# Kernel optimization log

Hardware: AMD Instinct MI355X
Metric: run time of the kernel (lower is better)

The kernel has to match this reference:

```python
import jax, jax.numpy as jnp
import numpy as np

NUM_HEADS = 8
GROUPS = 32
EPS = 1e-5


def setup_inputs() -> dict:
    key = jax.random.key(0)
    k1, k2, k3 = jax.random.split(key, 3)
    B, C, H, W = 16, 512, 64, 64
    x = jax.random.normal(k1, (B, C, H, W), dtype=jnp.float32)
    scale = C ** -0.5  # keep qkv/proj outputs well-scaled
    return {
        "x": x,
        "norm_w": jnp.ones((C,), jnp.float32),
        "norm_b": jnp.zeros((C,), jnp.float32),
        "qkv_w": jax.random.normal(k2, (3 * C, C), dtype=jnp.float32) * scale,
        "qkv_b": jnp.zeros((3 * C,), jnp.float32),
        "proj_w": jax.random.normal(k3, (C, C), dtype=jnp.float32) * scale,
        "proj_b": jnp.zeros((C,), jnp.float32),
    }


def reference(x, norm_w, norm_b, qkv_w, qkv_b, proj_w, proj_b):
    B, C, H, W = x.shape
    N = H * W
    nh = NUM_HEADS
    hd = C // nh

    # GroupNorm(32, C)
    xg = x.reshape(B, GROUPS, C // GROUPS, N)
    mu = xg.mean(axis=(2, 3), keepdims=True)
    var = xg.var(axis=(2, 3), keepdims=True)
    h = ((xg - mu) * jax.lax.rsqrt(var + EPS)).reshape(B, C, N)
    h = h * norm_w[None, :, None] + norm_b[None, :, None]

    h = h.transpose(0, 2, 1)  # [B, N, C]
    qkv = (h @ qkv_w.T + qkv_b).reshape(B, N, 3, nh, hd)
    q, k, v = qkv[:, :, 0], qkv[:, :, 1], qkv[:, :, 2]  # each [B, N, nh, hd]

    # Faithful to source: attention over the HEAD axis at each position
    attn = jnp.einsum('bnhd,bngd->bnhg', q, k) * (hd ** -0.5)  # [B, N, nh, nh]
    attn = jax.nn.softmax(attn, axis=-1)
    o = jnp.einsum('bnhg,bngd->bnhd', attn, v).reshape(B, N, C)

    o = o @ proj_w.T + proj_b  # [B, N, C]
    return x + o.transpose(0, 2, 1).reshape(B, C, H, W)
```

## Files before the change

kernel.cpp:

```cpp
#include <hip/hip_runtime.h>

typedef __attribute__((ext_vector_type(8))) short short8v;
typedef __attribute__((ext_vector_type(4))) float float4v;
typedef unsigned short ushortT;

__device__ __forceinline__ unsigned short f2bf(float f) {
  union { float f; unsigned u; } a; a.f = f;
  unsigned r = a.u + 0x7fffu + ((a.u >> 16) & 1u);
  return (unsigned short)(r >> 16);
}
__device__ __forceinline__ float2 up2(unsigned u) {
  union { unsigned u; float f; } a, b;
  a.u = u << 16; b.u = u & 0xffff0000u;
  return make_float2(a.f, b.f);
}
__device__ __forceinline__ void gl_lds16(const void* g, void* l) {
  __builtin_amdgcn_global_load_lds(
      (const __attribute__((address_space(1))) void*)g,
      (__attribute__((address_space(3))) void*)l, 16, 0, 0);
}

#define WAITV4 asm volatile("s_waitcnt vmcnt(4)" ::: "memory")
#define WAITV0 asm volatile("s_waitcnt vmcnt(0)" ::: "memory")
#define BAR()  __builtin_amdgcn_s_barrier()
#define MFMA16(d, a, b) d = __builtin_amdgcn_mfma_f32_16x16x32_bf16(a, b, d, 0, 0, 0)

__global__ __launch_bounds__(256) void prep(const float* __restrict__ qkvw,
                                            const float* __restrict__ pw,
                                            const float* __restrict__ x,
                                            ushortT* __restrict__ wq_b,
                                            ushortT* __restrict__ wp_b,
                                            float2* __restrict__ stats) {
  int bid = blockIdx.x, tid = threadIdx.x;
  if (bid < 1024) {
    const float* src = (bid < 768) ? qkvw : pw;
    ushortT* dst     = (bid < 768) ? wq_b : wp_b;
    int base = (bid < 768) ? bid : (bid - 768);
    int i = (base * 256 + tid) * 4;
    float4 v = *(const float4*)(src + i);
    uint2 o;
    o.x = (unsigned)f2bf(v.x) | ((unsigned)f2bf(v.y) << 16);
    o.y = (unsigned)f2bf(v.z) | ((unsigned)f2bf(v.w) << 16);
    *(uint2*)(dst + i) = o;
    return;
  }
  int bg = bid - 1024;
  const float* base = x + (size_t)bg * 65536;
  float s = 0.f, s2 = 0.f;
  for (int i = tid; i < 16384; i += 256) {
    float4 v = *(const float4*)(base + (size_t)i * 4);
    s  += v.x + v.y + v.z + v.w;
    s2 += v.x * v.x + v.y * v.y + v.z * v.z + v.w * v.w;
  }
  #pragma unroll
  for (int off = 32; off > 0; off >>= 1) {
    s  += __shfl_down(s, off);
    s2 += __shfl_down(s2, off);
  }
  __shared__ float red[8];
  int w = tid >> 6, l = tid & 63;
  if (l == 0) { red[w] = s; red[w + 4] = s2; }
  __syncthreads();
  if (tid == 0) {
    float ts = red[0] + red[1] + red[2] + red[3];
    float t2 = red[4] + red[5] + red[6] + red[7];
    float mean = ts * (1.f / 65536.f);
    float var  = t2 * (1.f / 65536.f) - mean * mean;
    stats[bg] = make_float2(mean, rsqrtf(var + 1e-5f));
  }
}

__global__ __launch_bounds__(512) void norm_tr(const float* __restrict__ x,
                                               const float* __restrict__ nw,
                                               const float* __restrict__ nb,
                                               const float2* __restrict__ stats,
                                               ushortT* __restrict__ h) {
  __shared__ float t[64][65];
  int n0 = blockIdx.x * 64, c0 = blockIdx.y * 64, b = blockIdx.z;
  int tx = threadIdx.x, ty = threadIdx.y;
  #pragma unroll
  for (int j = ty; j < 64; j += 8) {
    int c = c0 + j;
    float2 ms = stats[b * 32 + (c >> 4)];
    float v = x[((size_t)b * 512 + c) * 4096 + n0 + tx];
    t[j][tx] = (v - ms.x) * ms.y * nw[c] + nb[c];
  }
  __syncthreads();
  #pragma unroll
  for (int j = ty; j < 64; j += 8) {
    int n = n0 + j;
    h[((size_t)b * 4096 + n) * 512 + c0 + tx] = f2bf(t[tx][j]);
  }
}

__device__ __forceinline__ void core256b(const ushortT* __restrict__ A,
                                         const ushortT* __restrict__ Bm,
                                         ushortT* lds, int m0, int n0,
                                         float4v (&acc)[8][4]) {
  char* ldsb = (char*)lds;
  const int tid = threadIdx.x;
  const int w = tid >> 6, l = tid & 63;
  const int wm = w >> 2, wn = w & 3;

  const int P0b = tid * 16, P1b = 8192 + tid * 16;
  const int r0 = P0b >> 7, r1 = P1b >> 7;
  const int s0 = (P0b & 127) ^ ((r0 & 7) << 4);
  const int s1 = (P1b & 127) ^ ((r1 & 7) << 4);
  const size_t g0 = (size_t)r0 * 512 + (s0 >> 1);
  const size_t g1 = (size_t)r1 * 512 + (s1 >> 1);
  auto stage = [&](const ushortT* mat, int rowbase, int kt, int bufb, int region) {
    const ushortT* gsrc = mat + (size_t)rowbase * 512 + kt * 64;
    char* dbase = ldsb + bufb + region;
    gl_lds16(gsrc + g0, dbase + P0b);
    gl_lds16(gsrc + g1, dbase + P1b);
  };

  const int colb = (l >> 4) * 16;
  const int cs0 = colb ^ ((l & 7) << 4);
  const int cs1 = (64 + colb) ^ ((l & 7) << 4);
  const int arow = wm * 16384 + (l & 15) * 128;
  const int brow = 32768 + wn * 8192 + (l & 15) * 128;

  short8v Af[4][2], Bf[4][2];

  #define RDA4(bb, MH)                                                  \
    { _Pragma("unroll")                                                 \
      for (int mm = 0; mm < 4; ++mm) {                                  \
        const char* p = ldsb + (bb) + arow + ((MH)*4 + mm) * 2048;      \
        Af[mm][0] = *(const short8v*)(p + cs0);                         \
        Af[mm][1] = *(const short8v*)(p + cs1);                         \
      } }
  #define RDB2(bb, N0)                                                  \
    { _Pragma("unroll")                                                 \
      for (int nn = 0; nn < 2; ++nn) {                                  \
        const char* p = ldsb + (bb) + brow + ((N0) + nn) * 2048;        \
        Bf[(N0)+nn][0] = *(const short8v*)(p + cs0);                    \
        Bf[(N0)+nn][1] = *(const short8v*)(p + cs1);                    \
      } }
  #define CLUSTER(MH, NP)                                               \
    { __builtin_amdgcn_s_setprio(1);                                    \
      _Pragma("unroll")                                                 \
      for (int mm = 0; mm < 4; ++mm) {                                  \
        _Pragma("unroll")                                               \
        for (int nn = 0; nn < 2; ++nn) {                                \
          MFMA16(acc[(MH)*4+mm][(NP)*2+nn], Af[mm][0], Bf[(NP)*2+nn][0]); \
          MFMA16(acc[(MH)*4+mm][(NP)*2+nn], Af[mm][1], Bf[(NP)*2+nn][1]); \
        } }                                                             \
      __builtin_amdgcn_s_setprio(0); }

  auto tile = [&](int bb, int t1, int t2, bool s1g, bool s2g, int vw) {
    RDB2(bb, 0); RDA4(bb, 0);
    if (s1g) stage(A, m0 + 128, t1, bb ^ 65536, 16384);
    BAR();
    CLUSTER(0, 0);
    BAR();
    RDB2(bb, 2);
    if (s1g) stage(Bm, n0 + 128, t1, bb ^ 65536, 49152);
    BAR();
    CLUSTER(0, 1);
    BAR();
    RDA4(bb, 1);
    if (s2g) stage(Bm, n0, t2, bb, 32768);
    BAR();
    CLUSTER(1, 1);
    BAR();
    if (s2g) stage(A, m0, t2, bb, 0);
    if (vw == 4)      { WAITV4; }
    else if (vw == 0) { WAITV0; }
    BAR();
    CLUSTER(1, 0);
    BAR();
  };

  stage(A,  m0,       0, 0, 0);
  stage(A,  m0 + 128, 0, 0, 16384);
  stage(Bm, n0,       0, 0, 32768);
  stage(Bm, n0 + 128, 0, 0, 49152);
  stage(Bm, n0,       1, 65536, 32768);
  stage(A,  m0,       1, 65536, 0);
  WAITV4;
  BAR();

  #pragma unroll 1
  for (int tp = 0; tp < 3; ++tp) {
    tile(0,     2 * tp + 1, 2 * tp + 2, true, true, 4);
    tile(65536, 2 * tp + 2, 2 * tp + 3, true, true, 4);
  }
  tile(0,     7, 8, true,  false, 0);
  tile(65536, 8, 9, false, false, -1);
  #undef RDA4
  #undef RDB2
  #undef CLUSTER
}

__global__ __launch_bounds__(512, 2) void gemm_qkv(const ushortT* __restrict__ h,
                                                   const ushortT* __restrict__ wq,
                                                   const float* __restrict__ bias,
                                                   ushortT* __restrict__ outq) {
  __shared__ ushortT lds[65536];
  int bid = blockIdx.x;
  int wg = (bid & 7) * 192 + (bid >> 3);
  int m0 = (wg / 6) * 256, n0 = (wg % 6) * 256;
  float4v acc[8][4] = {};
  core256b(h, wq, lds, m0, n0, acc);
  const int tid = threadIdx.x;
  const int w = tid >> 6, l = tid & 63;
  const int wm = w >> 2, wn = w & 3;
  __syncthreads();
  ushortT* es = lds + w * 1280;
  float bb[4];
  #pragma unroll
  for (int fn = 0; fn < 4; ++fn) bb[fn] = bias[n0 + wn * 64 + fn * 16 + (l & 15)];
  int r = l >> 2, g = l & 3;
  #pragma unroll
  for (int fm = 0; fm < 8; ++fm) {
    #pragma unroll
    for (int fn = 0; fn < 4; ++fn)
      #pragma unroll
      for (int j = 0; j < 4; ++j)
        es[((l >> 4) * 4 + j) * 72 + fn * 16 + (l & 15)] = f2bf(acc[fm][fn][j] + bb[fn]);
    uint4 v0 = *(const uint4*)(es + r * 72 + g * 16);
    uint4 v1 = *(const uint4*)(es + r * 72 + g * 16 + 8);
    size_t mrow = (size_t)m0 + wm * 128 + fm * 16 + r;
    uint4* dst = (uint4*)(outq + mrow * 1536 + n0 + wn * 64 + g * 16);
    dst[0] = v0; dst[1] = v1;
  }
}

__global__ __launch_bounds__(256) void attn_k(const ushortT* __restrict__ qkv,
                                              ushortT* __restrict__ o) {
  __shared__ ushortT kv[16 * 1544];
  const int tid = threadIdx.x;
  const int p0 = blockIdx.x * 16;

  #pragma unroll
  for (int j = 0; j < 12; ++j) {
    int c = j * 256 + tid;
    int row = c / 192, col = c % 192;
    gl_lds16(qkv + (size_t)(p0 + row) * 1536 + col * 8,
             (char*)kv + row * 3088 + col * 16);
  }
  __syncthreads();

  const int pos = tid >> 4, h = (tid >> 1) & 7, dh = tid & 1;
  const ushortT* rowp = kv + pos * 1544;

  unsigned qv[16];
  {
    const uint4* qs = (const uint4*)(rowp + h * 64 + dh * 32);
    #pragma unroll
    for (int i = 0; i < 4; ++i) {
      uint4 u = qs[i];
      qv[i*4+0] = u.x; qv[i*4+1] = u.y; qv[i*4+2] = u.z; qv[i*4+3] = u.w;
    }
  }
  float lg[8];
  #pragma unroll
  for (int g = 0; g < 8; ++g) {
    const uint4* ks = (const uint4*)(rowp + 512 + g * 64 + dh * 32);
    float s = 0.f;
    #pragma unroll
    for (int i = 0; i < 4; ++i) {
      uint4 u = ks[i];
      float2 k0 = up2(u.x), k1 = up2(u.y), k2 = up2(u.z), k3 = up2(u.w);
      float2 q0 = up2(qv[i*4+0]), q1 = up2(qv[i*4+1]);
      float2 q2 = up2(qv[i*4+2]), q3 = up2(qv[i*4+3]);
      s += q0.x*k0.x + q0.y*k0.y + q1.x*k1.x + q1.y*k1.y
         + q2.x*k2.x + q2.y*k2.y + q3.x*k3.x + q3.y*k3.y;
    }
    s += __shfl_xor(s, 1);
    lg[g] = s * 0.125f;
  }
  float mx = lg[0];
  #pragma unroll
  for (int g = 1; g < 8; ++g) mx = fmaxf(mx, lg[g]);
  float ssum = 0.f;
  #pragma unroll
  for (int g = 0; g < 8; ++g) { lg[g] = __expf(lg[g] - mx); ssum += lg[g]; }
  float inv = 1.f / ssum;
  #pragma unroll
  for (int g = 0; g < 8; ++g) lg[g] *= inv;

  float oa[32];
  #pragma unroll
  for (int i = 0; i < 32; ++i) oa[i] = 0.f;
  #pragma unroll
  for (int g = 0; g < 8; ++g) {
    const uint4* vs = (const uint4*)(rowp + 1024 + g * 64 + dh * 32);
    float wg = lg[g];
    #pragma unroll
    for (int i = 0; i < 4; ++i) {
      uint4 u = vs[i];
      float2 v0 = up2(u.x), v1 = up2(u.y), v2 = up2(u.z), v3 = up2(u.w);
      oa[i*8+0] += wg*v0.x; oa[i*8+1] += wg*v0.y;
      oa[i*8+2] += wg*v1.x; oa[i*8+3] += wg*v1.y;
      oa[i*8+4] += wg*v2.x; oa[i*8+5] += wg*v2.y;
      oa[i*8+6] += wg*v3.x; oa[i*8+7] += wg*v3.y;
    }
  }
  ushortT* dst = o + (size_t)(p0 + pos) * 512 + h * 64 + dh * 32;
  #pragma unroll
  for (int i = 0; i < 4; ++i) {
    uint4 w_;
    w_.x = (unsigned)f2bf(oa[i*8+0]) | ((unsigned)f2bf(oa[i*8+1]) << 16);
    w_.y = (unsigned)f2bf(oa[i*8+2]) | ((unsigned)f2bf(oa[i*8+3]) << 16);
    w_.z = (unsigned)f2bf(oa[i*8+4]) | ((unsigned)f2bf(oa[i*8+5]) << 16);
    w_.w = (unsigned)f2bf(oa[i*8+6]) | ((unsigned)f2bf(oa[i*8+7]) << 16);
    *(uint4*)(dst + i * 8) = w_;
  }
}

__global__ __launch_bounds__(512, 2) void gemm_proj(const ushortT* __restrict__ o,
                                                    const ushortT* __restrict__ wp,
                                                    const float* __restrict__ bias,
                                                    const float* __restrict__ x,
                                                    float* __restrict__ out) {
  __shared__ ushortT lds[65536];
  int bid = blockIdx.x;
  int wg = (bid & 7) * 64 + (bid >> 3);
  int m0 = (wg >> 1) * 256, n0 = (wg & 1) * 256;
  float4v acc[8][4] = {};
  core256b(o, wp, lds, m0, n0, acc);
  const int tid = threadIdx.x;
  const int w = tid >> 6, l = tid & 63;
  const int wm = w >> 2, wn = w & 3;
  __syncthreads();
  float* es = (float*)((char*)lds + w * 4608);
  int b = m0 >> 12;
  int c = n0 + wn * 64 + l;
  float bc = bias[c];
  const float* xrow = x + ((size_t)b * 512 + c) * 4096;
  float* orow = out + ((size_t)b * 512 + c) * 4096;
  int nb0 = (m0 & 4095) + wm * 128;
  #pragma unroll
  for (int fm = 0; fm < 8; ++fm) {
    #pragma unroll
    for (int fn = 0; fn < 4; ++fn)
      #pragma unroll
      for (int j = 0; j < 4; ++j)
        es[((l >> 4) * 4 + j) * 68 + fn * 16 + (l & 15)] = acc[fm][fn][j];
    int nb = nb0 + fm * 16;
    #pragma unroll
    for (int q4 = 0; q4 < 4; ++q4) {
      float4 xv = *(const float4*)(xrow + nb + q4 * 4);
      float4 ov;
      ov.x = xv.x + bc + es[(q4 * 4 + 0) * 68 + l];
      ov.y = xv.y + bc + es[(q4 * 4 + 1) * 68 + l];
      ov.z = xv.z + bc + es[(q4 * 4 + 2) * 68 + l];
      ov.w = xv.w + bc + es[(q4 * 4 + 3) * 68 + l];
      *(float4*)(orow + nb + q4 * 4) = ov;
    }
  }
}

extern "C" void kernel_launch(void* const* d_in, const int* in_sizes, int n_in,
                              void* d_out, int out_size, void* d_ws, size_t ws_size,
                              hipStream_t stream) {
  const float* x     = (const float*)d_in[0];
  const float* nw    = (const float*)d_in[1];
  const float* nb    = (const float*)d_in[2];
  const float* qkvw  = (const float*)d_in[3];
  const float* qkvb  = (const float*)d_in[4];
  const float* pw    = (const float*)d_in[5];
  const float* pb    = (const float*)d_in[6];
  float* out = (float*)d_out;
  char* ws = (char*)d_ws;

  const size_t OFF_WQ   = 4096;
  const size_t OFF_WP   = OFF_WQ + 1572864;
  const size_t OFF_H    = OFF_WP + 524288;
  const size_t OFF_QKV  = OFF_H + 67108864;

  float2* stats   = (float2*)ws;
  ushortT* wq_b   = (ushortT*)(ws + OFF_WQ);
  ushortT* wp_b   = (ushortT*)(ws + OFF_WP);
  ushortT* h      = (ushortT*)(ws + OFF_H);
  ushortT* qkv    = (ushortT*)(ws + OFF_QKV);

  prep<<<1536, 256, 0, stream>>>(qkvw, pw, x, wq_b, wp_b, stats);
  norm_tr<<<dim3(64, 8, 16), dim3(64, 8), 0, stream>>>(x, nw, nb, stats, h);
  gemm_qkv<<<1536, 512, 0, stream>>>(h, wq_b, qkvb, qkv);
  attn_k<<<4096, 256, 0, stream>>>(qkv, h);
  gemm_proj<<<512, 512, 0, stream>>>(h, wp_b, pb, x, out);
}
```

Before: 367.9 us.

## Replace pipelined 256x256 GEMM core with simple 128x128 single-buffered tile

Replaces the double-buffered, barrier-scheduled 256x256 GEMM core with a 128x128 tile using 256 threads. It loads one 32-wide K slice per iteration into LDS and then runs the MFMAs. Block counts for the QKV and projection GEMMs grow four-fold to raise occupancy and parallelism. In exchange, the kernel loses global-load/compute overlap and does less operand reuse per byte loaded.

```diff
diff --git a/kernel.cpp b/kernel.cpp
--- a/kernel.cpp
+++ b/kernel.cpp
@@ -20,9 +20,6 @@
       (__attribute__((address_space(3))) void*)l, 16, 0, 0);
 }
 
-#define WAITV4 asm volatile("s_waitcnt vmcnt(4)" ::: "memory")
-#define WAITV0 asm volatile("s_waitcnt vmcnt(0)" ::: "memory")
-#define BAR()  __builtin_amdgcn_s_barrier()
 #define MFMA16(d, a, b) d = __builtin_amdgcn_mfma_f32_16x16x32_bf16(a, b, d, 0, 0, 0)
 
 __global__ __launch_bounds__(256) void prep(const float* __restrict__ qkvw,
@@ -93,135 +90,80 @@
   }
 }
 
-__device__ __forceinline__ void core256b(const ushortT* __restrict__ A,
-                                         const ushortT* __restrict__ Bm,
-                                         ushortT* lds, int m0, int n0,
-                                         float4v (&acc)[8][4]) {
+__device__ __forceinline__ void core128(const ushortT* __restrict__ A,
+                                        const ushortT* __restrict__ Bm,
+                                        ushortT* lds, int m0, int n0,
+                                        float4v (&acc)[4][4]) {
   char* ldsb = (char*)lds;
   const int tid = threadIdx.x;
   const int w = tid >> 6, l = tid & 63;
-  const int wm = w >> 2, wn = w & 3;
-
-  const int P0b = tid * 16, P1b = 8192 + tid * 16;
-  const int r0 = P0b >> 7, r1 = P1b >> 7;
-  const int s0 = (P0b & 127) ^ ((r0 & 7) << 4);
-  const int s1 = (P1b & 127) ^ ((r1 & 7) << 4);
-  const size_t g0 = (size_t)r0 * 512 + (s0 >> 1);
-  const size_t g1 = (size_t)r1 * 512 + (s1 >> 1);
-  auto stage = [&](const ushortT* mat, int rowbase, int kt, int bufb, int region) {
-    const ushortT* gsrc = mat + (size_t)rowbase * 512 + kt * 64;
-    char* dbase = ldsb + bufb + region;
-    gl_lds16(gsrc + g0, dbase + P0b);
-    gl_lds16(gsrc + g1, dbase + P1b);
-  };
-
-  const int colb = (l >> 4) * 16;
-  const int cs0 = colb ^ ((l & 7) << 4);
-  const int cs1 = (64 + colb) ^ ((l & 7) << 4);
-  const int arow = wm * 16384 + (l & 15) * 128;
-  const int brow = 32768 + wn * 8192 + (l & 15) * 128;
-
-  short8v Af[4][2], Bf[4][2];
-
-  #define RDA4(bb, MH)                                                  \
-    { _Pragma("unroll")                                                 \
-      for (int mm = 0; mm < 4; ++mm) {                                  \
-        const char* p = ldsb + (bb) + arow + ((MH)*4 + mm) * 2048;      \
-        Af[mm][0] = *(const short8v*)(p + cs0);                         \
-        Af[mm][1] = *(const short8v*)(p + cs1);                         \
-      } }
-  #define RDB2(bb, N0)                                                  \
-    { _Pragma("unroll")                                                 \
-      for (int nn = 0; nn < 2; ++nn) {                                  \
-        const char* p = ldsb + (bb) + brow + ((N0) + nn) * 2048;        \
-        Bf[(N0)+nn][0] = *(const short8v*)(p + cs0);                    \
-        Bf[(N0)+nn][1] = *(const short8v*)(p + cs1);                    \
-      } }
-  #define CLUSTER(MH, NP)                                               \
-    { __builtin_amdgcn_s_setprio(1);                                    \
-      _Pragma("unroll")                                                 \
-      for (int mm = 0; mm < 4; ++mm) {                                  \
-        _Pragma("unroll")                                               \
-        for (int nn = 0; nn < 2; ++nn) {                                \
-          MFMA16(acc[(MH)*4+mm][(NP)*2+nn], Af[mm][0], Bf[(NP)*2+nn][0]); \
-          MFMA16(acc[(MH)*4+mm][(NP)*2+nn], Af[mm][1], Bf[(NP)*2+nn][1]); \
-        } }                                                             \
-      __builtin_amdgcn_s_setprio(0); }
-
-  auto tile = [&](int bb, int t1, int t2, bool s1g, bool s2g, int vw) {
-    RDB2(bb, 0); RDA4(bb, 0);
-    if (s1g) stage(A, m0 + 128, t1, bb ^ 65536, 16384);
-    BAR();
-    CLUSTER(0, 0);
-    BAR();
-    RDB2(bb, 2);
-    if (s1g) stage(Bm, n0 + 128, t1, bb ^ 65536, 49152);
-    BAR();
-    CLUSTER(0, 1);
-    BAR();
-    RDA4(bb, 1);
-    if (s2g) stage(Bm, n0, t2, bb, 32768);
-    BAR();
-    CLUSTER(1, 1);
-    BAR();
-    if (s2g) stage(A, m0, t2, bb, 0);
-    if (vw == 4)      { WAITV4; }
-    else if (vw == 0) { WAITV0; }
-    BAR();
-    CLUSTER(1, 0);
-    BAR();
-  };
-
-  stage(A,  m0,       0, 0, 0);
-  stage(A,  m0 + 128, 0, 0, 16384);
-  stage(Bm, n0,       0, 0, 32768);
-  stage(Bm, n0 + 128, 0, 0, 49152);
-  stage(Bm, n0,       1, 65536, 32768);
-  stage(A,  m0,       1, 65536, 0);
-  WAITV4;
-  BAR();
+  const int wm = w >> 1, wn = w & 1;
+
+  const int r0 = tid >> 2, r1 = (256 + tid) >> 2;
+  const int s0 = (tid & 3) ^ ((r0 >> 1) & 3);
+  const int s1 = (tid & 3) ^ ((r1 >> 1) & 3);
+  const size_t gA0 = (size_t)r0 * 512 + s0 * 8;
+  const size_t gA1 = (size_t)r1 * 512 + s1 * 8;
+  const int d0 = tid * 16, d1 = (256 + tid) * 16;
+
+  const int cs = ((l >> 4) ^ (((l & 15) >> 1) & 3)) * 16;
+  const int ab = wm * 4096 + (l & 15) * 64 + cs;
+  const int bb = 8192 + wn * 4096 + (l & 15) * 64 + cs;
+
+  const ushortT* pa = A + (size_t)m0 * 512;
+  const ushortT* pb = Bm + (size_t)n0 * 512;
 
   #pragma unroll 1
-  for (int tp = 0; tp < 3; ++tp) {
-    tile(0,     2 * tp + 1, 2 * tp + 2, true, true, 4);
-    tile(65536, 2 * tp + 2, 2 * tp + 3, true, true, 4);
-  }
-  tile(0,     7, 8, true,  false, 0);
-  tile(65536, 8, 9, false, false, -1);
-  #undef RDA4
-  #undef RDB2
-  #undef CLUSTER
-}
-
-__global__ __launch_bounds__(512, 2) void gemm_qkv(const ushortT* __restrict__ h,
-                                                   const ushortT* __restrict__ wq,
-                                                   const float* __restrict__ bias,
-                                                   ushortT* __restrict__ outq) {
-  __shared__ ushortT lds[65536];
+  for (int kt = 0; kt < 16; ++kt) {
+    if (kt) __syncthreads();
+    gl_lds16(pa + gA0 + kt * 32, ldsb + d0);
+    gl_lds16(pa + gA1 + kt * 32, ldsb + d1);
+    gl_lds16(pb + gA0 + kt * 32, ldsb + 8192 + d0);
+    gl_lds16(pb + gA1 + kt * 32, ldsb + 8192 + d1);
+    __syncthreads();
+    short8v Af[4], Bf[4];
+    #pragma unroll
+    for (int i = 0; i < 4; ++i) {
+      Af[i] = *(const short8v*)(ldsb + ab + i * 1024);
+      Bf[i] = *(const short8v*)(ldsb + bb + i * 1024);
+    }
+    #pragma unroll
+    for (int mi = 0; mi < 4; ++mi)
+      #pragma unroll
+      for (int ni = 0; ni < 4; ++ni)
+        MFMA16(acc[mi][ni], Af[mi], Bf[ni]);
+  }
+}
+
+__global__ __launch_bounds__(256) void gemm_qkv(const ushortT* __restrict__ h,
+                                                const ushortT* __restrict__ wq,
+                                                const float* __restrict__ bias,
+                                                ushortT* __restrict__ outq) {
+  __shared__ ushortT lds[8192];
   int bid = blockIdx.x;
-  int wg = (bid & 7) * 192 + (bid >> 3);
-  int m0 = (wg / 6) * 256, n0 = (wg % 6) * 256;
-  float4v acc[8][4] = {};
-  core256b(h, wq, lds, m0, n0, acc);
+  int wg = (bid & 7) * 768 + (bid >> 3);
+  int m0 = (wg / 12) * 128, n0 = (wg % 12) * 128;
+  float4v acc[4][4] = {};
+  core128(h, wq, lds, m0, n0, acc);
   const int tid = threadIdx.x;
   const int w = tid >> 6, l = tid & 63;
-  const int wm = w >> 2, wn = w & 3;
+  const int wm = w >> 1, wn = w & 1;
   __syncthreads();
   ushortT* es = lds + w * 1280;
-  float bb[4];
-  #pragma unroll
-  for (int fn = 0; fn < 4; ++fn) bb[fn] = bias[n0 + wn * 64 + fn * 16 + (l & 15)];
+  float bb4[4];
+  #pragma unroll
+  for (int fn = 0; fn < 4; ++fn) bb4[fn] = bias[n0 + wn * 64 + fn * 16 + (l & 15)];
   int r = l >> 2, g = l & 3;
   #pragma unroll
-  for (int fm = 0; fm < 8; ++fm) {
+  for (int fm = 0; fm < 4; ++fm) {
     #pragma unroll
     for (int fn = 0; fn < 4; ++fn)
       #pragma unroll
       for (int j = 0; j < 4; ++j)
-        es[((l >> 4) * 4 + j) * 72 + fn * 16 + (l & 15)] = f2bf(acc[fm][fn][j] + bb[fn]);
+        es[((l >> 4) * 4 + j) * 72 + fn * 16 + (l & 15)] = f2bf(acc[fm][fn][j] + bb4[fn]);
     uint4 v0 = *(const uint4*)(es + r * 72 + g * 16);
     uint4 v1 = *(const uint4*)(es + r * 72 + g * 16 + 8);
-    size_t mrow = (size_t)m0 + wm * 128 + fm * 16 + r;
+    size_t mrow = (size_t)m0 + wm * 64 + fm * 16 + r;
     uint4* dst = (uint4*)(outq + mrow * 1536 + n0 + wn * 64 + g * 16);
     dst[0] = v0; dst[1] = v1;
   }
@@ -310,44 +252,44 @@
   }
 }
 
-__global__ __launch_bounds__(512, 2) void gemm_proj(const ushortT* __restrict__ o,
-                                                    const ushortT* __restrict__ wp,
-                                                    const float* __restrict__ bias,
-                                                    const float* __restrict__ x,
-                                                    float* __restrict__ out) {
-  __shared__ ushortT lds[65536];
+__global__ __launch_bounds__(256) void gemm_proj(const ushortT* __restrict__ o,
+                                                 const ushortT* __restrict__ wp,
+                                                 const float* __restrict__ bias,
+                                                 const float* __restrict__ x,
+                                                 float* __restrict__ out) {
+  __shared__ ushortT lds[8192];
   int bid = blockIdx.x;
-  int wg = (bid & 7) * 64 + (bid >> 3);
-  int m0 = (wg >> 1) * 256, n0 = (wg & 1) * 256;
-  float4v acc[8][4] = {};
-  core256b(o, wp, lds, m0, n0, acc);
+  int wg = (bid & 7) * 256 + (bid >> 3);
+  int m0 = (wg >> 2) * 128, n0 = (wg & 3) * 128;
+  float4v acc[4][4] = {};
+  core128(o, wp, lds, m0, n0, acc);
   const int tid = threadIdx.x;
   const int w = tid >> 6, l = tid & 63;
-  const int wm = w >> 2, wn = w & 3;
-  __syncthreads();
-  float* es = (float*)((char*)lds + w * 4608);
+  const int wm = w >> 1, wn = w & 1;
+  __syncthreads();
+  float* es = (float*)lds + w * 1024;
   int b = m0 >> 12;
   int c = n0 + wn * 64 + l;
   float bc = bias[c];
   const float* xrow = x + ((size_t)b * 512 + c) * 4096;
   float* orow = out + ((size_t)b * 512 + c) * 4096;
-  int nb0 = (m0 & 4095) + wm * 128;
-  #pragma unroll
-  for (int fm = 0; fm < 8; ++fm) {
+  int nb0 = (m0 & 4095) + wm * 64;
+  #pragma unroll
+  for (int fm = 0; fm < 4; ++fm) {
     #pragma unroll
     for (int fn = 0; fn < 4; ++fn)
       #pragma unroll
       for (int j = 0; j < 4; ++j)
-        es[((l >> 4) * 4 + j) * 68 + fn * 16 + (l & 15)] = acc[fm][fn][j];
+        es[((l >> 4) * 4 + j) * 64 + fn * 16 + (l & 15)] = acc[fm][fn][j];
     int nb = nb0 + fm * 16;
     #pragma unroll
     for (int q4 = 0; q4 < 4; ++q4) {
       float4 xv = *(const float4*)(xrow + nb + q4 * 4);
       float4 ov;
-      ov.x = xv.x + bc + es[(q4 * 4 + 0) * 68 + l];
-      ov.y = xv.y + bc + es[(q4 * 4 + 1) * 68 + l];
-      ov.z = xv.z + bc + es[(q4 * 4 + 2) * 68 + l];
-      ov.w = xv.w + bc + es[(q4 * 4 + 3) * 68 + l];
+      ov.x = xv.x + bc + es[(q4 * 4 + 0) * 64 + l];
+      ov.y = xv.y + bc + es[(q4 * 4 + 1) * 64 + l];
+      ov.z = xv.z + bc + es[(q4 * 4 + 2) * 64 + l];
+      ov.w = xv.w + bc + es[(q4 * 4 + 3) * 64 + l];
       *(float4*)(orow + nb + q4 * 4) = ov;
     }
   }
@@ -379,7 +321,7 @@
 
   prep<<<1536, 256, 0, stream>>>(qkvw, pw, x, wq_b, wp_b, stats);
   norm_tr<<<dim3(64, 8, 16), dim3(64, 8), 0, stream>>>(x, nw, nb, stats, h);
-  gemm_qkv<<<1536, 512, 0, stream>>>(h, wq_b, qkvb, qkv);
+  gemm_qkv<<<6144, 256, 0, stream>>>(h, wq_b, qkvb, qkv);
   attn_k<<<4096, 256, 0, stream>>>(qkv, h);
-  gemm_proj<<<512, 512, 0, stream>>>(h, wp_b, pb, x, out);
-}
+  gemm_proj<<<2048, 256, 0, stream>>>(h, wp_b, pb, x, out);
+}
```

Result: slower. 376.1 us (+2.2%).

## Use 128x128 tiles with a simple single-buffer core for proj GEMM

Applied to the files above, without the earlier changes.

Adds a 128x128 GEMM core that loads 32-wide K slices into 16KB of LDS with direct global-to-LDS loads, one barrier pair per K step, and 4x4 MFMA per wave. The projection GEMM switches from 512 blocks of 256x256 to 2048 blocks of 128x128 with 256 threads. The goal is more workgroups to fill the CUs, since 512 large tiles is a thin grid for 256 CUs. In exchange it drops the pipelined double-buffered schedule, so there is more global traffic per FLOP and barrier stalls are exposed. The epilogue stride also changes from 68 to 64, which may cause LDS bank conflicts.

```diff
diff --git a/kernel.cpp b/kernel.cpp
--- a/kernel.cpp
+++ b/kernel.cpp
@@ -193,6 +193,51 @@
   #undef CLUSTER
 }
 
+__device__ __forceinline__ void core128(const ushortT* __restrict__ A,
+                                        const ushortT* __restrict__ Bm,
+                                        ushortT* lds, int m0, int n0,
+                                        float4v (&acc)[4][4]) {
+  char* ldsb = (char*)lds;
+  const int tid = threadIdx.x;
+  const int w = tid >> 6, l = tid & 63;
+  const int wm = w >> 1, wn = w & 1;
+
+  const int r0 = tid >> 2, r1 = (256 + tid) >> 2;
+  const int s0 = (tid & 3) ^ ((r0 >> 1) & 3);
+  const int s1 = (tid & 3) ^ ((r1 >> 1) & 3);
+  const size_t gA0 = (size_t)r0 * 512 + s0 * 8;
+  const size_t gA1 = (size_t)r1 * 512 + s1 * 8;
+  const int d0 = tid * 16, d1 = (256 + tid) * 16;
+
+  const int cs = ((l >> 4) ^ (((l & 15) >> 1) & 3)) * 16;
+  const int ab = wm * 4096 + (l & 15) * 64 + cs;
+  const int bb = 8192 + wn * 4096 + (l & 15) * 64 + cs;
+
+  const ushortT* pa = A + (size_t)m0 * 512;
+  const ushortT* pb = Bm + (size_t)n0 * 512;
+
+  #pragma unroll 1
+  for (int kt = 0; kt < 16; ++kt) {
+    if (kt) __syncthreads();
+    gl_lds16(pa + gA0 + kt * 32, ldsb + d0);
+    gl_lds16(pa + gA1 + kt * 32, ldsb + d1);
+    gl_lds16(pb + gA0 + kt * 32, ldsb + 8192 + d0);
+    gl_lds16(pb + gA1 + kt * 32, ldsb + 8192 + d1);
+    __syncthreads();
+    short8v Af[4], Bf[4];
+    #pragma unroll
+    for (int i = 0; i < 4; ++i) {
+      Af[i] = *(const short8v*)(ldsb + ab + i * 1024);
+      Bf[i] = *(const short8v*)(ldsb + bb + i * 1024);
+    }
+    #pragma unroll
+    for (int mi = 0; mi < 4; ++mi)
+      #pragma unroll
+      for (int ni = 0; ni < 4; ++ni)
+        MFMA16(acc[mi][ni], Af[mi], Bf[ni]);
+  }
+}
+
 __global__ __launch_bounds__(512, 2) void gemm_qkv(const ushortT* __restrict__ h,
                                                    const ushortT* __restrict__ wq,
                                                    const float* __restrict__ bias,
@@ -310,44 +355,44 @@
   }
 }
 
-__global__ __launch_bounds__(512, 2) void gemm_proj(const ushortT* __restrict__ o,
-                                                    const ushortT* __restrict__ wp,
-                                                    const float* __restrict__ bias,
-                                                    const float* __restrict__ x,
-                                                    float* __restrict__ out) {
-  __shared__ ushortT lds[65536];
+__global__ __launch_bounds__(256) void gemm_proj(const ushortT* __restrict__ o,
+                                                 const ushortT* __restrict__ wp,
+                                                 const float* __restrict__ bias,
+                                                 const float* __restrict__ x,
+                                                 float* __restrict__ out) {
+  __shared__ ushortT lds[8192];
   int bid = blockIdx.x;
-  int wg = (bid & 7) * 64 + (bid >> 3);
-  int m0 = (wg >> 1) * 256, n0 = (wg & 1) * 256;
-  float4v acc[8][4] = {};
-  core256b(o, wp, lds, m0, n0, acc);
+  int wg = (bid & 7) * 256 + (bid >> 3);
+  int m0 = (wg >> 2) * 128, n0 = (wg & 3) * 128;
+  float4v acc[4][4] = {};
+  core128(o, wp, lds, m0, n0, acc);
   const int tid = threadIdx.x;
   const int w = tid >> 6, l = tid & 63;
-  const int wm = w >> 2, wn = w & 3;
+  const int wm = w >> 1, wn = w & 1;
   __syncthreads();
-  float* es = (float*)((char*)lds + w * 4608);
+  float* es = (float*)lds + w * 1024;
   int b = m0 >> 12;
   int c = n0 + wn * 64 + l;
   float bc = bias[c];
   const float* xrow = x + ((size_t)b * 512 + c) * 4096;
   float* orow = out + ((size_t)b * 512 + c) * 4096;
-  int nb0 = (m0 & 4095) + wm * 128;
-  #pragma unroll
-  for (int fm = 0; fm < 8; ++fm) {
+  int nb0 = (m0 & 4095) + wm * 64;
+  #pragma unroll
+  for (int fm = 0; fm < 4; ++fm) {
     #pragma unroll
     for (int fn = 0; fn < 4; ++fn)
       #pragma unroll
       for (int j = 0; j < 4; ++j)
-        es[((l >> 4) * 4 + j) * 68 + fn * 16 + (l & 15)] = acc[fm][fn][j];
+        es[((l >> 4) * 4 + j) * 64 + fn * 16 + (l & 15)] = acc[fm][fn][j];
     int nb = nb0 + fm * 16;
     #pragma unroll
     for (int q4 = 0; q4 < 4; ++q4) {
       float4 xv = *(const float4*)(xrow + nb + q4 * 4);
       float4 ov;
-      ov.x = xv.x + bc + es[(q4 * 4 + 0) * 68 + l];
-      ov.y = xv.y + bc + es[(q4 * 4 + 1) * 68 + l];
-      ov.z = xv.z + bc + es[(q4 * 4 + 2) * 68 + l];
-      ov.w = xv.w + bc + es[(q4 * 4 + 3) * 68 + l];
+      ov.x = xv.x + bc + es[(q4 * 4 + 0) * 64 + l];
+      ov.y = xv.y + bc + es[(q4 * 4 + 1) * 64 + l];
+      ov.z = xv.z + bc + es[(q4 * 4 + 2) * 64 + l];
+      ov.w = xv.w + bc + es[(q4 * 4 + 3) * 64 + l];
       *(float4*)(orow + nb + q4 * 4) = ov;
     }
   }
@@ -381,5 +426,5 @@
   norm_tr<<<dim3(64, 8, 16), dim3(64, 8), 0, stream>>>(x, nw, nb, stats, h);
   gemm_qkv<<<1536, 512, 0, stream>>>(h, wq_b, qkvb, qkv);
   attn_k<<<4096, 256, 0, stream>>>(qkv, h);
-  gemm_proj<<<512, 512, 0, stream>>>(h, wp_b, pb, x, out);
-}
+  gemm_proj<<<2048, 256, 0, stream>>>(h, wp_b, pb, x, out);
+}
```

Result: faster. 353.4 us, median of 2 (-3.9%).
